# Kernel tuning notes

Hardware: AMD Instinct MI355X
Metric: run time of the kernel (lower is better)

The kernel has to match this reference:

```python
import jax, jax.numpy as jnp
import numpy as np

SEQ_LEN = 128
IN_F = 16
OUT_F = 16
K_ORDER = 3
BATCH = 1024


def setup_inputs() -> dict:
    key = jax.random.key(0)
    k1, k2, k3 = jax.random.split(key, 3)
    x = jax.random.normal(k1, (BATCH, SEQ_LEN, IN_F), dtype=jnp.float32)
    # Glorot-uniform init for weight [k, in, out]
    lim = float(np.sqrt(6.0 / (IN_F + OUT_F)))
    weight = jax.random.uniform(k2, (K_ORDER, IN_F, OUT_F), dtype=jnp.float32, minval=-lim, maxval=lim)
    bias = jnp.zeros((OUT_F,), dtype=jnp.float32)
    adj_param = jax.random.normal(k3, (IN_F, IN_F), dtype=jnp.float32)
    return {"x": x, "weight": weight, "bias": bias, "adj_param": adj_param}


def _cheb_polynomials(adj_param, seq_len, in_f, k_order):
    """Vectorized build of the normalized-Laplacian Chebyshev basis.

    Replaces the original per-element Python loops:
      - temporal edges: node (i,f) <-> (i+1,f)  (symmetric shift by in_f)
      - feature edges : sigmoid(adj_param) off-diagonal, block-diag per time step
    """
    n = seq_len * in_f
    eye_n = jnp.eye(n, dtype=jnp.float32)
    # temporal edges
    offs = jnp.arange((seq_len - 1) * in_f)
    temporal = jnp.zeros((n, n), dtype=jnp.float32).at[offs, offs + in_f].set(1.0)
    temporal = temporal + temporal.T
    # feature edges (zero diagonal), replicated block-diagonally over time
    feat = jax.nn.sigmoid(adj_param) * (1.0 - jnp.eye(in_f, dtype=jnp.float32))
    adj = temporal + jnp.kron(jnp.eye(seq_len, dtype=jnp.float32), feat) + eye_n
    # symmetric normalization: L = I - D^{-1/2} A D^{-1/2}
    d = jnp.sum(adj, axis=1)
    d_inv_sqrt = jnp.where(d > 0, d ** -0.5, 0.0)
    lap = eye_n - d_inv_sqrt[:, None] * adj * d_inv_sqrt[None, :]
    # spectral rescale: L_scaled = 2/||L||_2 * L - I  (||.||_2 = largest singular value)
    l_scaled = (2.0 / jnp.linalg.norm(lap, ord=2)) * lap - eye_n
    polys = [eye_n, l_scaled]
    for _ in range(2, k_order):
        polys.append(2.0 * (l_scaled @ polys[-1]) - polys[-2])
    return polys


def reference(x, weight, bias, adj_param):
    batch, seq_len, in_f = x.shape
    k_order, _, out_f = weight.shape
    polys = _cheb_polynomials(adj_param, seq_len, in_f, k_order)
    x_flat = x.reshape(batch, seq_len * in_f)  # [B, N]
    out = jnp.zeros((batch, seq_len, out_f), dtype=x.dtype)
    for k in range(k_order):
        x_k = (x_flat @ polys[k]).reshape(batch, seq_len, in_f)
        out = out + jnp.einsum("bsf,fo->bso", x_k, weight[k])
    return out + bias
```

## Files before the change

### kernel.cpp

```cpp
#include <hip/hip_runtime.h>
#include <math.h>


#define MU_MIN (-1.99940694f)
#define C_OFF 163840

__device__ __forceinline__ float dot16(float x) {
  x += __shfl_xor(x, 1);
  x += __shfl_xor(x, 2);
  x += __shfl_xor(x, 4);
  x += __shfl_xor(x, 8);
  return x;
}

__global__ __launch_bounds__(256) void kS_sigma(const float* __restrict__ adj,
                                                float* __restrict__ wsf) {
  const int tid = threadIdx.x;
  __shared__ float Bsh[256];
  __shared__ float dis_i[16];
  __shared__ float H0[512], Pb[512], Qb[512];
  __shared__ float scl[2], lamsh[2];
  __shared__ int jst[2];

  {
    const int f = tid >> 4, g = tid & 15;
    const float a = adj[tid];
    const float s = 1.f / (1.f + expf(-a));
    Bsh[tid] = (f == g) ? 1.f : s;
  }
  __syncthreads();
  if (tid < 16) {
    float rs = 0.f;
    #pragma unroll
    for (int j = 0; j < 16; j++) rs += Bsh[tid * 16 + j];
    dis_i[tid] = rsqrtf(rs + 2.f);
  }
  __syncthreads();

  const int pass = tid >> 7, idx = tid & 127;
  const int pb = pass * 256;
  const float mu = pass ? -MU_MIN : MU_MIN;
  for (int e = idx; e < 256; e += 128) {
    const int f = e >> 4, g = e & 15;
    float gv = -dis_i[f] * Bsh[e] * dis_i[g];
    if (f == g) gv += 1.f - mu * dis_i[f] * dis_i[f];
    Pb[pb + e] = gv;
  }
  __syncthreads();
  for (int e = idx; e < 256; e += 128) {
    const int r = e >> 4, q = e & 15;
    float s = 0.f;
    #pragma unroll
    for (int k = 0; k < 16; k++) s += Pb[pb + k * 16 + r] * Pb[pb + k * 16 + q];
    H0[pb + e] = s;
    Qb[pb + e] = s;
  }
  __syncthreads();

  float* cur = Qb;
  float* nxt = Pb;
  #pragma unroll 1
  for (int it = 0; it < 8; it++) {
    if (idx == 0) {
      float tr = 0.f;
      #pragma unroll
      for (int d = 0; d < 16; d++) tr += cur[pb + d * 17];
      scl[pass] = 1.f / (tr * tr);
    }
    __syncthreads();
    const float s2 = scl[pass];
    for (int e = idx; e < 256; e += 128) {
      const int r = e >> 4, q = e & 15;
      const float4* rr = (const float4*)(cur + pb + r * 16);
      const float4* qq = (const float4*)(cur + pb + q * 16);
      float s = 0.f;
      #pragma unroll
      for (int k4 = 0; k4 < 4; k4++) {
        const float4 a = rr[k4], b = qq[k4];
        s += a.x * b.x + a.y * b.y + a.z * b.z + a.w * b.w;
      }
      nxt[pb + e] = s * s2;
    }
    __syncthreads();
    float* tmp = cur; cur = nxt; nxt = tmp;
  }
  if (idx == 0) {
    int bj = 0; float bd = -1.f;
    #pragma unroll
    for (int d = 0; d < 16; d++) {
      const float v = cur[pb + d * 17];
      if (v > bd) { bd = v; bj = d; }
    }
    jst[pass] = bj;
  }
  __syncthreads();
  if (idx < 16) {
    const int r = idx, js = jst[pass];
    const float vr = cur[pb + r * 16 + js];
    float hv = 0.f;
    #pragma unroll
    for (int q = 0; q < 16; q++) hv += H0[pb + r * 16 + q] * cur[pb + q * 16 + js];
    const float num = dot16(vr * hv);
    const float den = dot16(vr * vr);
    if (r == 0) lamsh[pass] = num / fmaxf(den, 1e-30f);
  }
  __syncthreads();
  if (tid == 0) {
    const float lam = fmaxf(fmaxf(lamsh[0], lamsh[1]), 1e-20f);
    wsf[C_OFF] = 2.f / sqrtf(lam);
  }
}

__global__ __launch_bounds__(256) void kM_build(const float* __restrict__ adj,
                                                const float* __restrict__ W,
                                                float* __restrict__ wsf) {
  const int t = blockIdx.x;
  const int tid = threadIdx.x;
  __shared__ float Bsh[256], Wsh[768];
  __shared__ float Dm[256], D0[256], Dp[256], DD[256];
  __shared__ float dis_i[16], dis_b[16], csh[1];

  {
    const int f = tid >> 4, g = tid & 15;
    const float a = adj[tid];
    const float s = 1.f / (1.f + expf(-a));
    Bsh[tid] = (f == g) ? 1.f : s;
    Wsh[tid] = W[tid];
    Wsh[tid + 256] = W[tid + 256];
    Wsh[tid + 512] = W[tid + 512];
    if (tid == 0) csh[0] = wsf[C_OFF];
  }
  __syncthreads();
  if (tid < 16) {
    float rs = 0.f;
    #pragma unroll
    for (int j = 0; j < 16; j++) rs += Bsh[tid * 16 + j];
    dis_i[tid] = rsqrtf(rs + 2.f);
    dis_b[tid] = rsqrtf(rs + 1.f);
  }
  __syncthreads();
  const float c = csh[0];
  const int r = tid >> 4, q = tid & 15;

  auto uat = [&](int a_, int ff) -> float {
    return (a_ == 0 || a_ == 127) ? dis_b[ff] : dis_i[ff];
  };

  D0[tid] = ((r == q) ? (c - 1.f) : 0.f) - c * uat(t, r) * uat(t, q) * Bsh[tid];
  if (t > 0)   Dm[tid] = ((r == q) ? (c - 1.f) : 0.f) - c * uat(t - 1, r) * uat(t - 1, q) * Bsh[tid];
  if (t < 127) Dp[tid] = ((r == q) ? (c - 1.f) : 0.f) - c * uat(t + 1, r) * uat(t + 1, q) * Bsh[tid];
  __syncthreads();
  {
    float s = 0.f;
    #pragma unroll
    for (int k = 0; k < 16; k++) s += D0[r * 16 + k] * D0[k * 16 + q];
    DD[tid] = s;
  }
  __syncthreads();

  const int fo = r;
  const int o = q;
  float m[5];
  const float ut_f = uat(t, fo);

  {
    float acc = Wsh[fo * 16 + o];
    const float diag0 = 2.f * c * c * ut_f * ut_f *
                        ((t > 0 ? uat(t - 1, fo) * uat(t - 1, fo) : 0.f) +
                         (t < 127 ? uat(t + 1, fo) * uat(t + 1, fo) : 0.f)) - 1.f;
    #pragma unroll
    for (int fp = 0; fp < 16; fp++) {
      acc += D0[fo * 16 + fp] * Wsh[256 + fp * 16 + o];
      const float p2 = 2.f * DD[fo * 16 + fp] + ((fo == fp) ? diag0 : 0.f);
      acc += p2 * Wsh[512 + fp * 16 + o];
    }
    m[2] = acc;
  }
  if (t < 127) {
    const float gf = -c * uat(t + 1, fo) * ut_f;
    float acc = gf * Wsh[256 + fo * 16 + o];
    #pragma unroll
    for (int fp = 0; fp < 16; fp++) {
      const float gq = -c * uat(t + 1, fp) * uat(t, fp);
      const float p2 = 2.f * (gf * D0[fo * 16 + fp] + Dp[fo * 16 + fp] * gq);
      acc += p2 * Wsh[512 + fp * 16 + o];
    }
    m[3] = acc;
  } else m[3] = 0.f;
  if (t > 0) {
    const float gf = -c * uat(t - 1, fo) * ut_f;
    float acc = gf * Wsh[256 + fo * 16 + o];
    #pragma unroll
    for (int fp = 0; fp < 16; fp++) {
      const float gq = -c * uat(t - 1, fp) * uat(t, fp);
      const float p2 = 2.f * (Dm[fo * 16 + fp] * gq + gf * D0[fo * 16 + fp]);
      acc += p2 * Wsh[512 + fp * 16 + o];
    }
    m[1] = acc;
  } else m[1] = 0.f;
  m[4] = (t < 126) ? (2.f * c * c * uat(t + 2, fo) * uat(t + 1, fo) * uat(t + 1, fo) * ut_f
                      * Wsh[512 + fo * 16 + o]) : 0.f;
  m[0] = (t > 1) ? (2.f * c * c * uat(t - 2, fo) * uat(t - 1, fo) * uat(t - 1, fo) * ut_f
                    * Wsh[512 + fo * 16 + o]) : 0.f;

  #pragma unroll
  for (int d5 = 0; d5 < 5; d5++)
    wsf[((size_t)(t * 5 + d5) * 16 + fo) * 16 + o] = m[d5];
}

__global__ __launch_bounds__(256) void k3_main(const float* __restrict__ x,
                                               const float* __restrict__ bias,
                                               const float* __restrict__ wsf,
                                               float* __restrict__ out) {
  const int tg = blockIdx.y, bg = blockIdx.x;
  const int t0 = tg * 16, b0 = bg * 16;
  const int tid = threadIdx.x;
  const int tl = tid >> 4, o = tid & 15;
  const int t = t0 + tl;

  float M[80];
  {
    const float* Mt = wsf + (size_t)t * 5 * 256;
    #pragma unroll
    for (int i = 0; i < 80; i++) M[i] = Mt[i * 16 + o];
  }
  const float bo = bias[o];

  __shared__ float xs[1600];

  for (int cc = 0; cc < 4; cc++) {
    __syncthreads();
    for (int idx = tid; idx < 320; idx += 256) {
      const int cb = idx / 80, rem = idx % 80;
      const int rrow = rem >> 2, qq = rem & 3;
      int gr = t0 - 2 + rrow;
      gr = gr < 0 ? 0 : (gr > 127 ? 127 : gr);
      const float4 v = *(const float4*)(x + ((size_t)(b0 + cc * 4 + cb) * 128 + gr) * 16 + qq * 4);
      *(float4*)(xs + cb * 400 + rrow * 20 + qq * 4) = v;
    }
    __syncthreads();
    #pragma unroll
    for (int cb = 0; cb < 4; cb++) {
      float acc0 = bo, acc1 = 0.f;
      #pragma unroll
      for (int dt = 0; dt < 5; dt++) {
        const float* xr = xs + cb * 400 + (tl + dt) * 20;
        const float4 xa = *(const float4*)(xr);
        const float4 xb = *(const float4*)(xr + 4);
        const float4 xc = *(const float4*)(xr + 8);
        const float4 xd = *(const float4*)(xr + 12);
        const float* Mp = M + dt * 16;
        acc0 += xa.x * Mp[0] + xa.y * Mp[1] + xa.z * Mp[2] + xa.w * Mp[3]
              + xb.x * Mp[4] + xb.y * Mp[5] + xb.z * Mp[6] + xb.w * Mp[7];
        acc1 += xc.x * Mp[8] + xc.y * Mp[9] + xc.z * Mp[10] + xc.w * Mp[11]
              + xd.x * Mp[12] + xd.y * Mp[13] + xd.z * Mp[14] + xd.w * Mp[15];
      }
      out[((size_t)(b0 + cc * 4 + cb) * 128 + t) * 16 + o] = acc0 + acc1;
    }
  }
}

extern "C" void kernel_launch(void* const* d_in, const int* in_sizes, int n_in,
                              void* d_out, int out_size, void* d_ws, size_t ws_size,
                              hipStream_t stream) {
  const float* x    = (const float*)d_in[0];
  const float* W    = (const float*)d_in[1];
  const float* bias = (const float*)d_in[2];
  const float* adj  = (const float*)d_in[3];
  float* out = (float*)d_out;
  float* wsf = (float*)d_ws;

  kS_sigma<<<dim3(1),   dim3(256), 0, stream>>>(adj, wsf);
  kM_build<<<dim3(128), dim3(256), 0, stream>>>(adj, W, wsf);
  k3_main<<<dim3(64, 8), dim3(256), 0, stream>>>(x, bias, wsf, out);
}
```

Measured before the change: 86.65 us.

## Fuse spectral-norm, operator build and main conv into one kernel with redundant per-block compute

Merges the three kernels into one launch in which every block redundantly runs the power-iteration spectral-norm estimate and builds only the banded operator matrices it needs. Interior time steps share a single operator and only the boundary blocks build extra ones. The operators are kept in shared memory, the global workspace round trip is dropped, and the first x tile is prefetched into registers before the setup work. This removes two launch boundaries and their serialization, at the cost of repeating the serial eigen-iteration in all 512 blocks and using much more shared memory per block.

Measured after the change: 86.92 us. Within noise of the previous version (+0.3%).

```diff
diff --git a/kernel.cpp b/kernel.cpp
--- a/kernel.cpp
+++ b/kernel.cpp
@@ -3,7 +3,7 @@
 
 
 #define MU_MIN (-1.99940694f)
-#define C_OFF 163840
+#define MSTRIDE 1300
 
 __device__ __forceinline__ float dot16(float x) {
   x += __shfl_xor(x, 1);
@@ -13,20 +13,51 @@
   return x;
 }
 
-__global__ __launch_bounds__(256) void kS_sigma(const float* __restrict__ adj,
-                                                float* __restrict__ wsf) {
+__global__ __launch_bounds__(256) void k_all(const float* __restrict__ adj,
+                                             const float* __restrict__ W,
+                                             const float* __restrict__ x,
+                                             const float* __restrict__ bias,
+                                             float* __restrict__ out) {
+  const int bg = blockIdx.x;
+  const int tg = blockIdx.y;
+  const int t0 = tg * 16, b0 = bg * 16;
   const int tid = threadIdx.x;
-  __shared__ float Bsh[256];
-  __shared__ float dis_i[16];
+
+  __shared__ float Bsh[256], Wsh[768];
+  __shared__ float dis_i[16], dis_b[16], csh[1];
   __shared__ float H0[512], Pb[512], Qb[512];
   __shared__ float scl[2], lamsh[2];
   __shared__ int jst[2];
+  __shared__ float Dint[256], Dbnd[256], DDint[256], DDbnd[256];
+  __shared__ float Msh[4 * MSTRIDE];
+  __shared__ float xs[1600];
+
+  float4 xpre0, xpre1;
+  {
+    const int idx = tid;
+    const int cb = idx / 80, rem = idx % 80;
+    const int rrow = rem >> 2, qq = rem & 3;
+    int gr = t0 - 2 + rrow;
+    gr = gr < 0 ? 0 : (gr > 127 ? 127 : gr);
+    xpre0 = *(const float4*)(x + ((size_t)(b0 + cb) * 128 + gr) * 16 + qq * 4);
+  }
+  if (tid < 64) {
+    const int idx = tid + 256;
+    const int cb = idx / 80, rem = idx % 80;
+    const int rrow = rem >> 2, qq = rem & 3;
+    int gr = t0 - 2 + rrow;
+    gr = gr < 0 ? 0 : (gr > 127 ? 127 : gr);
+    xpre1 = *(const float4*)(x + ((size_t)(b0 + cb) * 128 + gr) * 16 + qq * 4);
+  }
 
   {
     const int f = tid >> 4, g = tid & 15;
     const float a = adj[tid];
     const float s = 1.f / (1.f + expf(-a));
     Bsh[tid] = (f == g) ? 1.f : s;
+    Wsh[tid] = W[tid];
+    Wsh[tid + 256] = W[tid + 256];
+    Wsh[tid + 512] = W[tid + 512];
   }
   __syncthreads();
   if (tid < 16) {
@@ -34,6 +65,7 @@
     #pragma unroll
     for (int j = 0; j < 16; j++) rs += Bsh[tid * 16 + j];
     dis_i[tid] = rsqrtf(rs + 2.f);
+    dis_b[tid] = rsqrtf(rs + 1.f);
   }
   __syncthreads();
 
@@ -56,7 +88,6 @@
     Qb[pb + e] = s;
   }
   __syncthreads();
-
   float* cur = Qb;
   float* nxt = Pb;
   #pragma unroll 1
@@ -107,138 +138,134 @@
   __syncthreads();
   if (tid == 0) {
     const float lam = fmaxf(fmaxf(lamsh[0], lamsh[1]), 1e-20f);
-    wsf[C_OFF] = 2.f / sqrtf(lam);
-  }
-}
-
-__global__ __launch_bounds__(256) void kM_build(const float* __restrict__ adj,
-                                                const float* __restrict__ W,
-                                                float* __restrict__ wsf) {
-  const int t = blockIdx.x;
-  const int tid = threadIdx.x;
-  __shared__ float Bsh[256], Wsh[768];
-  __shared__ float Dm[256], D0[256], Dp[256], DD[256];
-  __shared__ float dis_i[16], dis_b[16], csh[1];
-
-  {
-    const int f = tid >> 4, g = tid & 15;
-    const float a = adj[tid];
-    const float s = 1.f / (1.f + expf(-a));
-    Bsh[tid] = (f == g) ? 1.f : s;
-    Wsh[tid] = W[tid];
-    Wsh[tid + 256] = W[tid + 256];
-    Wsh[tid + 512] = W[tid + 512];
-    if (tid == 0) csh[0] = wsf[C_OFF];
-  }
-  __syncthreads();
-  if (tid < 16) {
-    float rs = 0.f;
-    #pragma unroll
-    for (int j = 0; j < 16; j++) rs += Bsh[tid * 16 + j];
-    dis_i[tid] = rsqrtf(rs + 2.f);
-    dis_b[tid] = rsqrtf(rs + 1.f);
-  }
-  __syncthreads();
+    csh[0] = 2.f / sqrtf(lam);
+  }
+  __syncthreads();
+
   const float c = csh[0];
   const int r = tid >> 4, q = tid & 15;
-
+  Dint[tid] = ((r == q) ? (c - 1.f) : 0.f) - c * dis_i[r] * dis_i[q] * Bsh[tid];
+  Dbnd[tid] = ((r == q) ? (c - 1.f) : 0.f) - c * dis_b[r] * dis_b[q] * Bsh[tid];
+  __syncthreads();
+  {
+    float s0 = 0.f, s1 = 0.f;
+    #pragma unroll
+    for (int k = 0; k < 16; k++) {
+      s0 += Dint[r * 16 + k] * Dint[k * 16 + q];
+      s1 += Dbnd[r * 16 + k] * Dbnd[k * 16 + q];
+    }
+    DDint[tid] = s0;
+    DDbnd[tid] = s1;
+  }
+  __syncthreads();
+
+  int tvs[4], nv;
+  if (tg == 0)      { nv = 4; tvs[0] = 8; tvs[1] = 0;   tvs[2] = 1;   tvs[3] = 2;   }
+  else if (tg == 7) { nv = 4; tvs[0] = 8; tvs[1] = 125; tvs[2] = 126; tvs[3] = 127; }
+  else              { nv = 1; tvs[0] = 8; }
+
+  const int fo = r;
+  const int o = q;
   auto uat = [&](int a_, int ff) -> float {
     return (a_ == 0 || a_ == 127) ? dis_b[ff] : dis_i[ff];
   };
 
-  D0[tid] = ((r == q) ? (c - 1.f) : 0.f) - c * uat(t, r) * uat(t, q) * Bsh[tid];
-  if (t > 0)   Dm[tid] = ((r == q) ? (c - 1.f) : 0.f) - c * uat(t - 1, r) * uat(t - 1, q) * Bsh[tid];
-  if (t < 127) Dp[tid] = ((r == q) ? (c - 1.f) : 0.f) - c * uat(t + 1, r) * uat(t + 1, q) * Bsh[tid];
-  __syncthreads();
-  {
-    float s = 0.f;
-    #pragma unroll
-    for (int k = 0; k < 16; k++) s += D0[r * 16 + k] * D0[k * 16 + q];
-    DD[tid] = s;
-  }
-  __syncthreads();
-
-  const int fo = r;
-  const int o = q;
-  float m[5];
-  const float ut_f = uat(t, fo);
-
-  {
-    float acc = Wsh[fo * 16 + o];
-    const float diag0 = 2.f * c * c * ut_f * ut_f *
-                        ((t > 0 ? uat(t - 1, fo) * uat(t - 1, fo) : 0.f) +
-                         (t < 127 ? uat(t + 1, fo) * uat(t + 1, fo) : 0.f)) - 1.f;
-    #pragma unroll
-    for (int fp = 0; fp < 16; fp++) {
-      acc += D0[fo * 16 + fp] * Wsh[256 + fp * 16 + o];
-      const float p2 = 2.f * DD[fo * 16 + fp] + ((fo == fp) ? diag0 : 0.f);
-      acc += p2 * Wsh[512 + fp * 16 + o];
-    }
-    m[2] = acc;
-  }
-  if (t < 127) {
-    const float gf = -c * uat(t + 1, fo) * ut_f;
-    float acc = gf * Wsh[256 + fo * 16 + o];
-    #pragma unroll
-    for (int fp = 0; fp < 16; fp++) {
-      const float gq = -c * uat(t + 1, fp) * uat(t, fp);
-      const float p2 = 2.f * (gf * D0[fo * 16 + fp] + Dp[fo * 16 + fp] * gq);
-      acc += p2 * Wsh[512 + fp * 16 + o];
-    }
-    m[3] = acc;
-  } else m[3] = 0.f;
-  if (t > 0) {
-    const float gf = -c * uat(t - 1, fo) * ut_f;
-    float acc = gf * Wsh[256 + fo * 16 + o];
-    #pragma unroll
-    for (int fp = 0; fp < 16; fp++) {
-      const float gq = -c * uat(t - 1, fp) * uat(t, fp);
-      const float p2 = 2.f * (Dm[fo * 16 + fp] * gq + gf * D0[fo * 16 + fp]);
-      acc += p2 * Wsh[512 + fp * 16 + o];
-    }
-    m[1] = acc;
-  } else m[1] = 0.f;
-  m[4] = (t < 126) ? (2.f * c * c * uat(t + 2, fo) * uat(t + 1, fo) * uat(t + 1, fo) * ut_f
+  #pragma unroll 1
+  for (int v = 0; v < nv; v++) {
+    const int t = tvs[v];
+    const float* D0p = (t == 0 || t == 127) ? Dbnd : Dint;
+    const float* Dmp = (t == 1)   ? Dbnd : Dint;
+    const float* Dpp = (t == 126) ? Dbnd : Dint;
+    const float* DDp = (t == 0 || t == 127) ? DDbnd : DDint;
+    float m[5];
+    const float ut_f = uat(t, fo);
+
+    {
+      float acc = Wsh[fo * 16 + o];
+      const float diag0 = 2.f * c * c * ut_f * ut_f *
+                          ((t > 0 ? uat(t - 1, fo) * uat(t - 1, fo) : 0.f) +
+                           (t < 127 ? uat(t + 1, fo) * uat(t + 1, fo) : 0.f)) - 1.f;
+      #pragma unroll
+      for (int fp = 0; fp < 16; fp++) {
+        acc += D0p[fo * 16 + fp] * Wsh[256 + fp * 16 + o];
+        const float p2 = 2.f * DDp[fo * 16 + fp] + ((fo == fp) ? diag0 : 0.f);
+        acc += p2 * Wsh[512 + fp * 16 + o];
+      }
+      m[2] = acc;
+    }
+    if (t < 127) {
+      const float gf = -c * uat(t + 1, fo) * ut_f;
+      float acc = gf * Wsh[256 + fo * 16 + o];
+      #pragma unroll
+      for (int fp = 0; fp < 16; fp++) {
+        const float gq = -c * uat(t + 1, fp) * uat(t, fp);
+        acc += 2.f * (gf * D0p[fo * 16 + fp] + Dpp[fo * 16 + fp] * gq) * Wsh[512 + fp * 16 + o];
+      }
+      m[3] = acc;
+    } else m[3] = 0.f;
+    if (t > 0) {
+      const float gf = -c * uat(t - 1, fo) * ut_f;
+      float acc = gf * Wsh[256 + fo * 16 + o];
+      #pragma unroll
+      for (int fp = 0; fp < 16; fp++) {
+        const float gq = -c * uat(t - 1, fp) * uat(t, fp);
+        acc += 2.f * (Dmp[fo * 16 + fp] * gq + gf * D0p[fo * 16 + fp]) * Wsh[512 + fp * 16 + o];
+      }
+      m[1] = acc;
+    } else m[1] = 0.f;
+    m[4] = (t < 126) ? (2.f * c * c * uat(t + 2, fo) * uat(t + 1, fo) * uat(t + 1, fo) * ut_f
+                        * Wsh[512 + fo * 16 + o]) : 0.f;
+    m[0] = (t > 1) ? (2.f * c * c * uat(t - 2, fo) * uat(t - 1, fo) * uat(t - 1, fo) * ut_f
                       * Wsh[512 + fo * 16 + o]) : 0.f;
-  m[0] = (t > 1) ? (2.f * c * c * uat(t - 2, fo) * uat(t - 1, fo) * uat(t - 1, fo) * ut_f
-                    * Wsh[512 + fo * 16 + o]) : 0.f;
-
-  #pragma unroll
-  for (int d5 = 0; d5 < 5; d5++)
-    wsf[((size_t)(t * 5 + d5) * 16 + fo) * 16 + o] = m[d5];
-}
-
-__global__ __launch_bounds__(256) void k3_main(const float* __restrict__ x,
-                                               const float* __restrict__ bias,
-                                               const float* __restrict__ wsf,
-                                               float* __restrict__ out) {
-  const int tg = blockIdx.y, bg = blockIdx.x;
-  const int t0 = tg * 16, b0 = bg * 16;
-  const int tid = threadIdx.x;
-  const int tl = tid >> 4, o = tid & 15;
+
+    float* Mv = Msh + v * MSTRIDE;
+    #pragma unroll
+    for (int d5 = 0; d5 < 5; d5++)
+      Mv[d5 * 256 + fo * 16 + o] = m[d5];
+  }
+
+  {
+    const int cb = tid / 80, rem = tid % 80;
+    const int rrow = rem >> 2, qq = rem & 3;
+    *(float4*)(xs + cb * 400 + rrow * 20 + qq * 4) = xpre0;
+  }
+  if (tid < 64) {
+    const int idx2 = tid + 256;
+    const int cb = idx2 / 80, rem = idx2 % 80;
+    const int rrow = rem >> 2, qq = rem & 3;
+    *(float4*)(xs + cb * 400 + rrow * 20 + qq * 4) = xpre1;
+  }
+  __syncthreads();
+
+  const int tl = r;
   const int t = t0 + tl;
-
+  int vm = 0;
+  if (tg == 0)      vm = (tl < 3)  ? tl + 1  : 0;
+  else if (tg == 7) vm = (tl > 12) ? tl - 12 : 0;
   float M[80];
   {
-    const float* Mt = wsf + (size_t)t * 5 * 256;
-    #pragma unroll
-    for (int i = 0; i < 80; i++) M[i] = Mt[i * 16 + o];
+    const float* Mv = Msh + vm * MSTRIDE;
+    #pragma unroll
+    for (int dt = 0; dt < 5; dt++)
+      #pragma unroll
+      for (int f = 0; f < 16; f++)
+        M[dt * 16 + f] = Mv[dt * 256 + f * 16 + o];
   }
   const float bo = bias[o];
 
-  __shared__ float xs[1600];
-
   for (int cc = 0; cc < 4; cc++) {
-    __syncthreads();
-    for (int idx = tid; idx < 320; idx += 256) {
-      const int cb = idx / 80, rem = idx % 80;
-      const int rrow = rem >> 2, qq = rem & 3;
-      int gr = t0 - 2 + rrow;
-      gr = gr < 0 ? 0 : (gr > 127 ? 127 : gr);
-      const float4 v = *(const float4*)(x + ((size_t)(b0 + cc * 4 + cb) * 128 + gr) * 16 + qq * 4);
-      *(float4*)(xs + cb * 400 + rrow * 20 + qq * 4) = v;
-    }
-    __syncthreads();
+    if (cc > 0) {
+      __syncthreads();
+      for (int ix = tid; ix < 320; ix += 256) {
+        const int cb = ix / 80, rem = ix % 80;
+        const int rrow = rem >> 2, qq = rem & 3;
+        int gr = t0 - 2 + rrow;
+        gr = gr < 0 ? 0 : (gr > 127 ? 127 : gr);
+        const float4 vv = *(const float4*)(x + ((size_t)(b0 + cc * 4 + cb) * 128 + gr) * 16 + qq * 4);
+        *(float4*)(xs + cb * 400 + rrow * 20 + qq * 4) = vv;
+      }
+      __syncthreads();
+    }
     #pragma unroll
     for (int cb = 0; cb < 4; cb++) {
       float acc0 = bo, acc1 = 0.f;
@@ -268,9 +295,7 @@
   const float* bias = (const float*)d_in[2];
   const float* adj  = (const float*)d_in[3];
   float* out = (float*)d_out;
-  float* wsf = (float*)d_ws;
-
-  kS_sigma<<<dim3(1),   dim3(256), 0, stream>>>(adj, wsf);
-  kM_build<<<dim3(128), dim3(256), 0, stream>>>(adj, W, wsf);
-  k3_main<<<dim3(64, 8), dim3(256), 0, stream>>>(x, bias, wsf, out);
+  (void)d_ws; (void)ws_size;
+
+  k_all<<<dim3(64, 8), dim3(256), 0, stream>>>(adj, W, x, bias, out);
 }
```
